# Performance work log

Hardware: AMD Instinct MI355X
Metric: run time of the kernel (lower is better)

Reference implementation:

```python
import jax, jax.numpy as jnp
from jax import lax
import numpy as np

NGF = 64
NZ = 16
B, H, W = 4, 224, 224
CTX = 512
HEADS = 1

def _gauss_kernel():
    ks, sigma = 3, 1.0
    ax = np.arange(ks, dtype=np.float32)
    xg, yg = np.meshgrid(ax, ax)
    mean = (ks - 1) / 2.0
    k = np.exp(-((xg - mean) ** 2 + (yg - mean) ** 2) / (2.0 * sigma ** 2)) / (2.0 * np.pi * sigma ** 2)
    k = k / k.sum()
    return jnp.asarray(np.tile(k[None, None], (3, 1, 1, 1)).astype(np.float32))

_GK = _gauss_kernel()  # depthwise gaussian blur kernel [3,1,3,3]

def _conv(x, w, stride=1, pad=0, groups=1):
    return lax.conv_general_dilated(x, w, (stride, stride), ((pad, pad), (pad, pad)),
                                    feature_group_count=groups,
                                    dimension_numbers=('NCHW', 'OIHW', 'NCHW'))

def _convT(x, w):
    # torch ConvTranspose2d(k=3, stride=2, padding=1, output_padding=1)
    wt = jnp.flip(w, (2, 3)).transpose(1, 0, 2, 3)
    return lax.conv_general_dilated(x, wt, (1, 1), ((1, 2), (1, 2)), lhs_dilation=(2, 2),
                                    dimension_numbers=('NCHW', 'OIHW', 'NCHW'))

def _refl(x, p):
    return jnp.pad(x, ((0, 0), (0, 0), (p, p), (p, p)), mode='reflect')

def _bn(x, g, b):
    # eval-mode BatchNorm2d with running_mean=0, running_var=1, eps=1e-5
    inv = g / np.float32(np.sqrt(1.0 + 1e-5))
    return x * inv[None, :, None, None] + b[None, :, None, None]

def _gn(x, g, b, groups=32, eps=1e-6):
    bsz, c, h, w = x.shape
    xr = x.reshape(bsz, groups, c // groups, h, w)
    m = xr.mean((2, 3, 4), keepdims=True)
    v = xr.var((2, 3, 4), keepdims=True)
    xr = (xr - m) / jnp.sqrt(v + eps)
    return xr.reshape(bsz, c, h, w) * g[None, :, None, None] + b[None, :, None, None]

def _ln(x, g, b, eps=1e-5):
    m = x.mean(-1, keepdims=True)
    v = x.var(-1, keepdims=True)
    return (x - m) / jnp.sqrt(v + eps) * g + b

def _attn(xq, ctx, wq, wk, wv, wo, bo, heads=HEADS):
    d = wq.shape[0] // heads
    scale = d ** -0.5
    q = xq @ wq.T
    k = ctx @ wk.T
    v = ctx @ wv.T
    bsz, n, _ = q.shape
    m = k.shape[1]
    q = q.reshape(bsz, n, heads, d).transpose(0, 2, 1, 3)
    k = k.reshape(bsz, m, heads, d).transpose(0, 2, 1, 3)
    v = v.reshape(bsz, m, heads, d).transpose(0, 2, 1, 3)
    sim = jnp.einsum('bhid,bhjd->bhij', q, k) * scale  # full score matrix, as in source
    a = jax.nn.softmax(sim, axis=-1)
    o = jnp.einsum('bhij,bhjd->bhid', a, v).transpose(0, 2, 1, 3).reshape(bsz, n, heads * d)
    return o @ wo.T + bo

def setup_inputs():
    keys = iter(jax.random.split(jax.random.key(0), 80))
    def rn(shape, s=0.02):
        return jax.random.normal(next(keys), shape, jnp.float32) * s
    c4 = NGF * 4
    d = {}
    d['input'] = jax.random.normal(next(keys), (B, 3, H, W), jnp.float32)
    d['cond'] = jax.random.normal(next(keys), (B, CTX), jnp.float32)
    d['sn_w'] = rn((NZ, CTX))
    d['sn_u'] = jax.random.normal(next(keys), (NZ,), jnp.float32)
    d['c1_w'] = rn((NGF, 3 + NZ, 7, 7))
    d['bn1_g'] = jnp.ones((NGF,)); d['bn1_b'] = jnp.zeros((NGF,))
    d['c2_w'] = rn((NGF * 2, NGF + NZ, 3, 3))
    d['bn2_g'] = jnp.ones((NGF * 2,)); d['bn2_b'] = jnp.zeros((NGF * 2,))
    d['c3_w'] = rn((c4, NGF * 2 + NZ, 3, 3))
    d['bn3_g'] = jnp.ones((c4,)); d['bn3_b'] = jnp.zeros((c4,))
    d['res_w'] = rn((6, 2, c4, c4, 3, 3))
    d['res_g'] = jnp.ones((6, 2, c4)); d['res_b'] = jnp.zeros((6, 2, c4))
    d['st_gn_g'] = jnp.ones((2, c4)); d['st_gn_b'] = jnp.zeros((2, c4))
    d['st_pin_w'] = rn((2, c4, c4, 1, 1)); d['st_pin_b'] = jnp.zeros((2, c4))
    d['st_q1'] = rn((2, c4, c4)); d['st_k1'] = rn((2, c4, c4)); d['st_v1'] = rn((2, c4, c4))
    d['st_o1w'] = rn((2, c4, c4)); d['st_o1b'] = jnp.zeros((2, c4))
    d['st_q2'] = rn((2, c4, c4)); d['st_k2'] = rn((2, c4, CTX)); d['st_v2'] = rn((2, c4, CTX))
    d['st_o2w'] = rn((2, c4, c4)); d['st_o2b'] = jnp.zeros((2, c4))
    d['st_ffp_w'] = rn((2, c4 * 8, c4)); d['st_ffp_b'] = jnp.zeros((2, c4 * 8))
    d['st_ffo_w'] = rn((2, c4, c4 * 4)); d['st_ffo_b'] = jnp.zeros((2, c4))
    for n in ('ln1', 'ln2', 'ln3'):
        d['st_' + n + 'g'] = jnp.ones((2, c4)); d['st_' + n + 'b'] = jnp.zeros((2, c4))
    d['st_pout_w'] = rn((2, c4, c4, 1, 1)); d['st_pout_b'] = jnp.zeros((2, c4))
    d['up1_w'] = rn((c4, NGF * 2, 3, 3))
    d['up1_g'] = jnp.ones((NGF * 2,)); d['up1_b'] = jnp.zeros((NGF * 2,))
    d['up2_w'] = rn((NGF * 2, NGF, 3, 3))
    d['up2_g'] = jnp.ones((NGF,)); d['up2_b'] = jnp.zeros((NGF,))
    d['cf_w'] = rn((3, NGF, 7, 7)); d['cf_b'] = jnp.zeros((3,))
    d['eps'] = 16
    return d

def reference(input, cond, eps, sn_w, sn_u, c1_w, bn1_g, bn1_b, c2_w, bn2_g, bn2_b, c3_w, bn3_g, bn3_b,
              res_w, res_g, res_b, st_gn_g, st_gn_b, st_pin_w, st_pin_b,
              st_q1, st_k1, st_v1, st_o1w, st_o1b, st_q2, st_k2, st_v2, st_o2w, st_o2b,
              st_ffp_w, st_ffp_b, st_ffo_w, st_ffo_b,
              st_ln1g, st_ln1b, st_ln2g, st_ln2b, st_ln3g, st_ln3b,
              st_pout_w, st_pout_b, up1_w, up1_g, up1_b, up2_w, up2_g, up2_b, cf_w, cf_b):
    relu = jax.nn.relu
    text_cond = cond[:, None, :]  # [B, 1, 512]
    # spectral-norm linear (one power iteration, u/v detached, as torch train-mode)
    v = sn_w.T @ sn_u
    v = v / (jnp.linalg.norm(v) + 1e-12)
    u = sn_w @ v
    u = u / (jnp.linalg.norm(u) + 1e-12)
    v = lax.stop_gradient(v); u = lax.stop_gradient(u)
    sigma = u @ (sn_w @ v)
    z = cond @ (sn_w / sigma).T  # [B, NZ]

    def tile_z(h, w):
        return jnp.broadcast_to(z[:, :, None, None], (z.shape[0], z.shape[1], h, w))

    x = jnp.concatenate([input, tile_z(input.shape[2], input.shape[3])], axis=1)
    x = relu(_bn(_conv(_refl(x, 3), c1_w), bn1_g, bn1_b))
    x = jnp.concatenate([x, tile_z(x.shape[2], x.shape[3])], axis=1)
    x = relu(_bn(_conv(x, c2_w, stride=2, pad=1), bn2_g, bn2_b))
    x = jnp.concatenate([x, tile_z(x.shape[2], x.shape[3])], axis=1)
    x = relu(_bn(_conv(x, c3_w, stride=2, pad=1), bn3_g, bn3_b))

    def resblock(x, w, g, b):
        h = relu(_bn(_conv(_refl(x, 1), w[0]), g[0], b[0]))  # dropout inactive (eval)
        h = _bn(_conv(_refl(h, 1), w[1]), g[1], b[1])
        return x + h

    def spatial_transformer(x, i):
        x_in = x
        x = _gn(x, st_gn_g[i], st_gn_b[i])
        x = _conv(x, st_pin_w[i]) + st_pin_b[i][None, :, None, None]
        bsz, c, h, w = x.shape
        t = x.reshape(bsz, c, h * w).transpose(0, 2, 1)  # b, hw, c
        h1 = _ln(t, st_ln1g[i], st_ln1b[i])
        t = _attn(h1, h1, st_q1[i], st_k1[i], st_v1[i], st_o1w[i], st_o1b[i]) + t
        h2 = _ln(t, st_ln2g[i], st_ln2b[i])
        t = _attn(h2, text_cond, st_q2[i], st_k2[i], st_v2[i], st_o2w[i], st_o2b[i]) + t
        h3 = _ln(t, st_ln3g[i], st_ln3b[i])
        p = h3 @ st_ffp_w[i].T + st_ffp_b[i]
        a, gate = jnp.split(p, 2, axis=-1)  # GEGLU
        t = (a * jax.nn.gelu(gate, approximate=False)) @ st_ffo_w[i].T + st_ffo_b[i] + t
        x = t.transpose(0, 2, 1).reshape(bsz, c, h, w)
        x = _conv(x, st_pout_w[i]) + st_pout_b[i][None, :, None, None]
        return x + x_in

    x = resblock(x, res_w[0], res_g[0], res_b[0])
    x = resblock(x, res_w[1], res_g[1], res_b[1])
    x = spatial_transformer(x, 0)
    x = resblock(x, res_w[2], res_g[2], res_b[2])
    x = resblock(x, res_w[3], res_g[3], res_b[3])
    x = spatial_transformer(x, 1)
    x = resblock(x, res_w[4], res_g[4], res_b[4])
    x = resblock(x, res_w[5], res_g[5], res_b[5])
    x = relu(_bn(_convT(x, up1_w), up1_g, up1_b))
    x = relu(_bn(_convT(x, up2_w), up2_g, up2_b))
    x = _conv(_refl(x, 3), cf_w) + cf_b[None, :, None, None]
    x = jnp.tanh(x)
    x = _conv(x, _GK, pad=1, groups=3)  # fixed gaussian blur
    return x * eps
```

## Files before the change

### kernel.cpp

```cpp
#include <hip/hip_runtime.h>
#include <math.h>

#ifndef DIVUP
#define DIVUP(a,b) (((a)+(b)-1)/(b))
#endif

typedef unsigned short ushort_t;
typedef __attribute__((ext_vector_type(8))) short v8s;
typedef __attribute__((ext_vector_type(4))) float v4f;

#define BB 4
#define NZ 16
#define C4 256
#define N56 3136
#define N112 12544
#define N224 50176

static const float BN_ALPHA = 0.99999500003749967f;

__device__ inline int refl_idx(int i, int n) {
  if (i < 0) i = -i;
  if (i >= n) i = 2 * n - 2 - i;
  return i;
}

__device__ inline void bsplit(float v, ushort_t& h, ushort_t& l) {
  unsigned b = __float_as_uint(v);
  unsigned r = (b + 0x7FFFu + ((b >> 16) & 1u)) & 0xFFFF0000u;
  h = (ushort_t)(r >> 16);
  float lo = v - __uint_as_float(r);
  unsigned bl_ = __float_as_uint(lo);
  unsigned rl = bl_ + 0x7FFFu + ((bl_ >> 16) & 1u);
  l = (ushort_t)(rl >> 16);
}

__device__ inline float blk_reduce_sum(float v, float* lds) {
  int t = threadIdx.x;
  lds[t] = v; __syncthreads();
  for (int s = 128; s > 0; s >>= 1) { if (t < s) lds[t] += lds[t + s]; __syncthreads(); }
  float r = lds[0]; __syncthreads();
  return r;
}
__device__ inline float blk_reduce_max(float v, float* lds) {
  int t = threadIdx.x;
  lds[t] = v; __syncthreads();
  for (int s = 128; s > 0; s >>= 1) { if (t < s) lds[t] = fmaxf(lds[t], lds[t + s]); __syncthreads(); }
  float r = lds[0]; __syncthreads();
  return r;
}

struct MArgs {
  const float* A; long long Am, Ak, Abatch;
  const float* Xp; long long Xbatch;
  const float* z;
  const ushort_t* Bh; const ushort_t* Bl;
  const float* Bf; long long Bbatch;
  long long Bstride;
  float* C; long long Cm, Cn, Cbatch;
  const float* scale; const float* bias;
  const float* resid; long long Rm, Rn, Rbatch;
  float alpha; int relu;
  int M, N;
  int ICP, NPH;
  int Cin;
  int KS, Hin, Win, Wout, stride, pad, reflect;
};

template<int AMODE, int BMN, int KSTEP, int BSPLIT>
__global__ __launch_bounds__(256, (BMN == 64 ? 3 : 2)) void mg_k(MArgs g) {
  constexpr int EPT  = BMN * KSTEP / 256;
  constexpr int MF   = BMN / 32;
  constexpr int LDSW = KSTEP + 8;
  constexpr int NSUB = KSTEP / 32;
  __shared__ __align__(16) ushort_t sAh[BMN * LDSW];
  __shared__ __align__(16) ushort_t sAl[BMN * LDSW];
  __shared__ __align__(16) ushort_t sBh[BMN * LDSW];
  __shared__ __align__(16) ushort_t sBl[BMN * LDSW];

  const int tid = threadIdx.x;
  const int b = blockIdx.z;
  const int m0 = blockIdx.y * BMN, n0 = blockIdx.x * BMN;
  const int lane = tid & 63, w = tid >> 6;
  const int wm = (w >> 1) * (MF * 16), wn = (w & 1) * (MF * 16);

  const int srow = tid & (BMN - 1);
  const int skoff = (tid / BMN) * EPT;

  int am = m0 + srow; if (am >= g.M) am = g.M - 1;
  int cy = 0, cx = 0;
  const float* Aptr;
  if (AMODE == 0) {
    Aptr = g.A + (long long)b * g.Abatch + (long long)am * g.Am;
  } else {
    cy = am / g.Wout; cx = am - cy * g.Wout;
    Aptr = g.Xp + (long long)b * g.Xbatch;
  }
  const int HW = g.Hin * g.Win;

  int bn = n0 + srow; if (bn >= g.N) bn = g.N - 1;
  const ushort_t* BhP = BSPLIT ? (g.Bh + (long long)bn * g.Bstride + skoff) : nullptr;
  const ushort_t* BlP = BSPLIT ? (g.Bl + (long long)bn * g.Bstride + skoff) : nullptr;
  const float* BfP = BSPLIT ? nullptr : (g.Bf + (long long)b * g.Bbatch + (long long)bn * g.Bstride + skoff);

  int ph = 0, ic0 = 0, pbase = 0;
  bool pvalid = true;
  int kglob = 0;

  float areg[EPT];
  ushort_t bregh[EPT], bregl[EPT];
  float bregf[EPT];

  auto fetchA = [&]() {
    if (AMODE == 0) {
      const float* Ap = Aptr + (long long)(kglob + skoff) * g.Ak;
      if (g.Ak == 1) {
        #pragma unroll
        for (int e = 0; e < EPT; ++e) areg[e] = Ap[e];
      } else {
        #pragma unroll
        for (int e = 0; e < EPT; ++e) areg[e] = Ap[(long long)e * g.Ak];
      }
      kglob += KSTEP;
    } else {
      if (ic0 == 0) {
        int ky = ph / g.KS, kx = ph - ky * g.KS;
        if (AMODE == 1) {
          int iy = cy * g.stride + ky - g.pad;
          int ix = cx * g.stride + kx - g.pad;
          if (g.reflect) {
            iy = refl_idx(iy, g.Hin); ix = refl_idx(ix, g.Win); pvalid = true;
          } else {
            pvalid = (iy >= 0 && iy < g.Hin && ix >= 0 && ix < g.Win);
            if (iy < 0) iy = 0; if (iy >= g.Hin) iy = g.Hin - 1;
            if (ix < 0) ix = 0; if (ix >= g.Win) ix = g.Win - 1;
          }
          pbase = iy * g.Win + ix;
        } else {
          int iy2 = cy + ky - 1, ix2 = cx + kx - 1;
          pvalid = (iy2 >= 0) && (ix2 >= 0) && !(iy2 & 1) && !(ix2 & 1);
          int iy = iy2 >> 1, ix = ix2 >> 1;
          if (pvalid && (iy >= g.Hin || ix >= g.Win)) pvalid = false;
          if (!pvalid) { iy = 0; ix = 0; }
          pbase = iy * g.Win + ix;
        }
      }
      #pragma unroll
      for (int e = 0; e < EPT; ++e) {
        int ic = ic0 + skoff + e;
        float v = 0.f;
        if (pvalid) {
          if (ic < g.Cin) v = Aptr[pbase + ic * HW];
          else if (g.z && ic < g.Cin + NZ) v = g.z[b * NZ + (ic - g.Cin)];
        }
        areg[e] = v;
      }
      ic0 += KSTEP; if (ic0 == g.ICP) { ic0 = 0; ++ph; }
    }
  };

  auto fetchB = [&](int k0) {
    if (BSPLIT) {
      #pragma unroll
      for (int e = 0; e < EPT; ++e) { bregh[e] = BhP[k0 + e]; bregl[e] = BlP[k0 + e]; }
    } else {
      #pragma unroll
      for (int e = 0; e < EPT; ++e) bregf[e] = BfP[k0 + e];
    }
  };

  v4f acc[MF][MF];
  #pragma unroll
  for (int i = 0; i < MF; ++i)
    #pragma unroll
    for (int j = 0; j < MF; ++j) acc[i][j] = (v4f)(0.f);

  const int nt = (g.ICP * g.NPH) / KSTEP;
  fetchA(); fetchB(0);

  const int fr = lane & 15, fk = (lane >> 4) * 8;

  for (int t = 0; t < nt; ++t) {
    __syncthreads();
    {
      ushort_t ah[EPT], al[EPT];
      #pragma unroll
      for (int e = 0; e < EPT; ++e) bsplit(areg[e], ah[e], al[e]);
      #pragma unroll
      for (int e = 0; e < EPT; ++e) { sAh[srow * LDSW + skoff + e] = ah[e]; sAl[srow * LDSW + skoff + e] = al[e]; }
      if (BSPLIT) {
        #pragma unroll
        for (int e = 0; e < EPT; ++e) { sBh[srow * LDSW + skoff + e] = bregh[e]; sBl[srow * LDSW + skoff + e] = bregl[e]; }
      } else {
        ushort_t bh[EPT], bl[EPT];
        #pragma unroll
        for (int e = 0; e < EPT; ++e) bsplit(bregf[e], bh[e], bl[e]);
        #pragma unroll
        for (int e = 0; e < EPT; ++e) { sBh[srow * LDSW + skoff + e] = bh[e]; sBl[srow * LDSW + skoff + e] = bl[e]; }
      }
    }
    __syncthreads();
    if (t + 1 < nt) { fetchA(); fetchB((t + 1) * KSTEP); }
    #pragma unroll
    for (int ks = 0; ks < NSUB; ++ks) {
      v8s fah[MF], fal[MF], fbh[MF], fbl[MF];
      #pragma unroll
      for (int i = 0; i < MF; ++i) {
        fah[i] = *(const v8s*)&sAh[(wm + i * 16 + fr) * LDSW + ks * 32 + fk];
        fal[i] = *(const v8s*)&sAl[(wm + i * 16 + fr) * LDSW + ks * 32 + fk];
        fbh[i] = *(const v8s*)&sBh[(wn + i * 16 + fr) * LDSW + ks * 32 + fk];
        fbl[i] = *(const v8s*)&sBl[(wn + i * 16 + fr) * LDSW + ks * 32 + fk];
      }
      #pragma unroll
      for (int i = 0; i < MF; ++i)
        #pragma unroll
        for (int j = 0; j < MF; ++j) {
          acc[i][j] = __builtin_amdgcn_mfma_f32_16x16x32_bf16(fah[i], fbh[j], acc[i][j], 0, 0, 0);
          acc[i][j] = __builtin_amdgcn_mfma_f32_16x16x32_bf16(fah[i], fbl[j], acc[i][j], 0, 0, 0);
          acc[i][j] = __builtin_amdgcn_mfma_f32_16x16x32_bf16(fal[i], fbh[j], acc[i][j], 0, 0, 0);
        }
    }
  }

  const int fq = lane >> 4;
  #pragma unroll
  for (int j = 0; j < MF; ++j) {
    int n = n0 + wn + j * 16 + fr;
    if (n >= g.N) continue;
    float sc = (g.scale ? g.scale[n] : 1.f) * g.alpha;
    float bs = g.bias ? g.bias[n] : 0.f;
    #pragma unroll
    for (int i = 0; i < MF; ++i) {
      int mb = m0 + wm + i * 16 + fq * 4;
      #pragma unroll
      for (int r = 0; r < 4; ++r) {
        int m = mb + r;
        if (m < g.M) {
          float v = acc[i][j][r] * sc + bs;
          if (g.resid) v += g.resid[(long long)b * g.Rbatch + (long long)m * g.Rm + (long long)n * g.Rn];
          if (g.relu) v = fmaxf(v, 0.f);
          g.C[(long long)b * g.Cbatch + (long long)m * g.Cm + (long long)n * g.Cn] = v;
        }
      }
    }
  }
}

__global__ void prep_lin_k(const float* __restrict__ src, ushort_t* __restrict__ dh,
                           ushort_t* __restrict__ dl, int tot) {
  int i = blockIdx.x * 256 + threadIdx.x;
  if (i >= tot) return;
  bsplit(src[i], dh[i], dl[i]);
}

__global__ void prep_conv_k(const float* __restrict__ src, ushort_t* __restrict__ dh,
                            ushort_t* __restrict__ dl, int N, int Cin, int ICP, int KS) {
  int idx = blockIdx.x * 256 + threadIdx.x;
  int K2 = KS * KS;
  int tot = N * K2 * ICP;
  if (idx >= tot) return;
  int ic = idx % ICP;
  int p = (idx / ICP) % K2;
  int n = idx / (ICP * K2);
  float v = (ic < Cin) ? src[(n * Cin + ic) * K2 + p] : 0.f;
  bsplit(v, dh[idx], dl[idx]);
}

__global__ void prep_convt_k(const float* __restrict__ src, ushort_t* __restrict__ dh,
                             ushort_t* __restrict__ dl, int Cin, int Cout) {
  int idx = blockIdx.x * 256 + threadIdx.x;
  int tot = Cout * 9 * Cin;
  if (idx >= tot) return;
  int ic = idx % Cin;
  int p = (idx / Cin) % 9;
  int o = idx / (9 * Cin);
  int ky = p / 3, kx = p % 3;
  float v = src[((ic * Cout + o) * 3 + (2 - ky)) * 3 + (2 - kx)];
  bsplit(v, dh[idx], dl[idx]);
}

__global__ __launch_bounds__(256) void spectral_z_k(const float* __restrict__ cond,
    const float* __restrict__ W, const float* __restrict__ u0, float* __restrict__ z) {
  __shared__ float v0[512];
  __shared__ float lds[256];
  __shared__ float wv[16];
  __shared__ float invs[2];
  int tid = threadIdx.x;
  float part = 0.f;
  #pragma unroll
  for (int r = 0; r < 2; ++r) {
    int j = tid + r * 256;
    float s = 0.f;
    #pragma unroll
    for (int i = 0; i < 16; ++i) s = fmaf(W[i * 512 + j], u0[i], s);
    v0[j] = s;
    part = fmaf(s, s, part);
  }
  float nv2 = blk_reduce_sum(part, lds);
  if (tid == 0) invs[0] = 1.f / (sqrtf(nv2) + 1e-12f);
  __syncthreads();
  float inv_nv = invs[0];
  {
    int i = tid >> 4, l = tid & 15;
    float s = 0.f;
    for (int jj = 0; jj < 32; ++jj) {
      int j = l + jj * 16;
      s = fmaf(W[i * 512 + j], v0[j], s);
    }
    lds[tid] = s; __syncthreads();
    if (l == 0) {
      float t = 0.f;
      for (int q = 0; q < 16; ++q) t += lds[(i << 4) + q];
      wv[i] = t * inv_nv;
    }
    __syncthreads();
    if (tid == 0) {
      float s2 = 0.f;
      for (int i2 = 0; i2 < 16; ++i2) s2 = fmaf(wv[i2], wv[i2], s2);
      float nw = sqrtf(s2);
      float sigma = s2 / (nw + 1e-12f);
      invs[1] = 1.f / sigma;
    }
    __syncthreads();
  }
  if (tid < 64) {
    int b = tid >> 4, i = tid & 15;
    float s = 0.f;
    for (int j = 0; j < 512; ++j) s = fmaf(cond[b * 512 + j], W[i * 512 + j], s);
    z[b * 16 + i] = s * invs[1];
  }
}

__global__ __launch_bounds__(256) void groupnorm_k(const float* __restrict__ x, float* __restrict__ out,
    const float* __restrict__ gam, const float* __restrict__ bet, int C, int HW, int cpg) {
  __shared__ float lds[256];
  int b = blockIdx.y, grp = blockIdx.x;
  long long base = ((long long)b * C + (long long)grp * cpg) * HW;
  int n = cpg * HW;
  float s = 0.f, s2 = 0.f;
  for (int i = threadIdx.x; i < n; i += 256) { float v = x[base + i]; s += v; s2 = fmaf(v, v, s2); }
  s  = blk_reduce_sum(s, lds);
  s2 = blk_reduce_sum(s2, lds);
  float m = s / (float)n;
  float var = s2 / (float)n - m * m;
  float rinv = 1.f / sqrtf(var + 1e-6f);
  for (int i = threadIdx.x; i < n; i += 256) {
    int c = grp * cpg + i / HW;
    out[base + i] = (x[base + i] - m) * rinv * gam[c] + bet[c];
  }
}

__global__ __launch_bounds__(256) void layernorm_k(const float* __restrict__ x, float* __restrict__ out,
    const float* __restrict__ g, const float* __restrict__ b) {
  __shared__ float lds[256];
  long long t = blockIdx.x;
  float v = x[t * 256 + threadIdx.x];
  float s  = blk_reduce_sum(v, lds);
  float s2 = blk_reduce_sum(v * v, lds);
  float m = s * (1.f / 256.f);
  float var = s2 * (1.f / 256.f) - m * m;
  float rinv = 1.f / sqrtf(var + 1e-5f);
  out[t * 256 + threadIdx.x] = (v - m) * rinv * g[threadIdx.x] + b[threadIdx.x];
}

__global__ __launch_bounds__(256) void softmax_k(float* __restrict__ S, float* __restrict__ den, int n) {
  __shared__ float lds[256];
  float* p = S + (long long)blockIdx.x * n;
  float mx = -3.4e38f;
  for (int i = threadIdx.x; i < n; i += 256) mx = fmaxf(mx, p[i]);
  mx = blk_reduce_max(mx, lds);
  float s = 0.f;
  for (int i = threadIdx.x; i < n; i += 256) { float e = __expf(p[i] - mx); p[i] = e; s += e; }
  s = blk_reduce_sum(s, lds);
  if (threadIdx.x == 0) den[blockIdx.x] = 1.f / s;
}

__global__ __launch_bounds__(256) void pv_reduce_k(const float* __restrict__ part,
    const float* __restrict__ den, float* __restrict__ out, int nchunk) {
  long long i = (long long)blockIdx.x * 256 + threadIdx.x;
  float s = 0.f;
  for (int c = 0; c < nchunk; ++c) s += part[(long long)c * 802816 + i];
  out[i] = s * den[i >> 8];
}

__global__ void geglu_k(float* __restrict__ p, int ntok) {
  int idx = blockIdx.x * 256 + threadIdx.x;
  if (idx >= ntok * 1024) return;
  int t = idx >> 10, j = idx & 1023;
  float a  = p[t * 2048 + j];
  float gt = p[t * 2048 + 1024 + j];
  float ge = 0.5f * gt * (1.f + erff(gt * 0.70710678118654752f));
  p[t * 2048 + j] = a * ge;
}

__global__ __launch_bounds__(256) void crossattn_vec_k(const float* __restrict__ cond,
    const float* __restrict__ v2w, const float* __restrict__ o2w, const float* __restrict__ o2b,
    float* __restrict__ o2buf) {
  __shared__ float kv[256];
  int b = blockIdx.x, oc = threadIdx.x;
  float s = 0.f;
  for (int j = 0; j < 512; ++j) s = fmaf(cond[b * 512 + j], v2w[oc * 512 + j], s);
  kv[oc] = s; __syncthreads();
  float o = o2b[oc];
  for (int ic = 0; ic < 256; ++ic) o = fmaf(kv[ic], o2w[oc * 256 + ic], o);
  o2buf[b * 256 + oc] = o;
}
__global__ void bcast_add_k(float* __restrict__ T, const float* __restrict__ o2buf, int ntok_per_b) {
  long long idx = (long long)blockIdx.x * 256 + threadIdx.x;
  int c = (int)(idx & 255);
  long long tb = idx >> 8;
  int b = (int)(tb / ntok_per_b);
  T[idx] += o2buf[b * 256 + c];
}

__global__ __launch_bounds__(256) void conv_final_k(const float* __restrict__ in,
    const float* __restrict__ w, const float* __restrict__ bias, float* __restrict__ out) {
  __shared__ float wl[3 * 64 * 49];
  for (int i = threadIdx.x; i < 3 * 64 * 49; i += 256) wl[i] = w[i];
  __syncthreads();
  int b = blockIdx.y;
  int p = blockIdx.x * 256 + threadIdx.x;
  int y = p / 224, x = p % 224;
  int iy[7], ix[7];
  #pragma unroll
  for (int t = 0; t < 7; ++t) {
    int a = y + t - 3; iy[t] = (a < 0) ? -a : ((a >= 224) ? 446 - a : a);
    int c = x + t - 3; ix[t] = (c < 0) ? -c : ((c >= 224) ? 446 - c : c);
  }
  float a0 = bias[0], a1 = bias[1], a2 = bias[2];
  for (int ic = 0; ic < 64; ++ic) {
    const float* ip = in + (long long)(b * 64 + ic) * N224;
    const float* w0 = &wl[(0 * 64 + ic) * 49];
    const float* w1 = &wl[(1 * 64 + ic) * 49];
    const float* w2 = &wl[(2 * 64 + ic) * 49];
    #pragma unroll
    for (int ky = 0; ky < 7; ++ky) {
      const float* rp = ip + iy[ky] * 224;
      #pragma unroll
      for (int kx = 0; kx < 7; ++kx) {
        float v = rp[ix[kx]];
        int t = ky * 7 + kx;
        a0 = fmaf(v, w0[t], a0);
        a1 = fmaf(v, w1[t], a1);
        a2 = fmaf(v, w2[t], a2);
      }
    }
  }
  long long ob = (long long)b * 3 * N224 + p;
  out[ob]            = tanhf(a0);
  out[ob + N224]     = tanhf(a1);
  out[ob + 2 * N224] = tanhf(a2);
}

__global__ void blur_k(const float* __restrict__ x, float* __restrict__ out, const int* __restrict__ epsp) {
  int idx = blockIdx.x * 256 + threadIdx.x;
  int xp = idx % 224;
  int y  = (idx / 224) % 224;
  int bc = idx / N224;
  const float* p = x + (long long)bc * N224;
  const float kc = 0.20417996f, k1 = 0.12384140f, k2 = 0.07511360f;
  float s = 0.f;
  #pragma unroll
  for (int dy = -1; dy <= 1; ++dy) {
    int yy = y + dy;
    if (yy < 0 || yy >= 224) continue;
    #pragma unroll
    for (int dx = -1; dx <= 1; ++dx) {
      int xx = xp + dx;
      if (xx < 0 || xx >= 224) continue;
      float wgt = (dy == 0 && dx == 0) ? kc : ((dy != 0 && dx != 0) ? k2 : k1);
      s = fmaf(p[yy * 224 + xx], wgt, s);
    }
  }
  out[idx] = s * (float)epsp[0];
}

static inline MArgs MA() { MArgs g = {}; g.alpha = 1.f; return g; }

template<int AMODE, int BMN, int KSTEP, int BSPLIT>
static inline void mgl(hipStream_t s, const MArgs& g, int zb) {
  dim3 grid(DIVUP(g.N, BMN), DIVUP(g.M, BMN), zb);
  mg_k<AMODE, BMN, KSTEP, BSPLIT><<<grid, 256, 0, s>>>(g);
}

extern "C" void kernel_launch(void* const* d_in, const int* in_sizes, int n_in,
                              void* d_out, int out_size, void* d_ws, size_t ws_size,
                              hipStream_t stream) {
  (void)in_sizes; (void)n_in; (void)out_size; (void)ws_size;
  const float* input = (const float*)d_in[0];
  const float* cond  = (const float*)d_in[1];
  const float* sn_w  = (const float*)d_in[2];
  const float* sn_u  = (const float*)d_in[3];
  const float* c1_w  = (const float*)d_in[4];
  const float* bn1_g = (const float*)d_in[5];
  const float* bn1_b = (const float*)d_in[6];
  const float* c2_w  = (const float*)d_in[7];
  const float* bn2_g = (const float*)d_in[8];
  const float* bn2_b = (const float*)d_in[9];
  const float* c3_w  = (const float*)d_in[10];
  const float* bn3_g = (const float*)d_in[11];
  const float* bn3_b = (const float*)d_in[12];
  const float* res_w = (const float*)d_in[13];
  const float* res_g = (const float*)d_in[14];
  const float* res_b = (const float*)d_in[15];
  const float* gn_g  = (const float*)d_in[16];
  const float* gn_b  = (const float*)d_in[17];
  const float* pin_w = (const float*)d_in[18];
  const float* pin_b = (const float*)d_in[19];
  const float* q1w   = (const float*)d_in[20];
  const float* k1w   = (const float*)d_in[21];
  const float* v1w   = (const float*)d_in[22];
  const float* o1w   = (const float*)d_in[23];
  const float* o1b   = (const float*)d_in[24];
  const float* v2w   = (const float*)d_in[27];
  const float* o2w   = (const float*)d_in[28];
  const float* o2b   = (const float*)d_in[29];
  const float* ffpw  = (const float*)d_in[30];
  const float* ffpb  = (const float*)d_in[31];
  const float* ffow  = (const float*)d_in[32];
  const float* ffob  = (const float*)d_in[33];
  const float* ln1g  = (const float*)d_in[34];
  const float* ln1b  = (const float*)d_in[35];
  const float* ln3g  = (const float*)d_in[38];
  const float* ln3b  = (const float*)d_in[39];
  const float* poutw = (const float*)d_in[40];
  const float* poutb = (const float*)d_in[41];
  const float* up1w  = (const float*)d_in[42];
  const float* up1g  = (const float*)d_in[43];
  const float* up1b  = (const float*)d_in[44];
  const float* up2w  = (const float*)d_in[45];
  const float* up2g  = (const float*)d_in[46];
  const float* up2b  = (const float*)d_in[47];
  const float* cfw   = (const float*)d_in[48];
  const float* cfb   = (const float*)d_in[49];
  const int*   epsp  = (const int*)d_in[50];

  const long long S56 = (long long)C4 * N56;

  float* A1   = (float*)d_ws;
  float* A2   = A1 + 12845056;
  float* SIMb = A2 + 6422528;
  float* X    = SIMb + 9834496;
  float* T    = X + 3211264;
  float* Hb   = T + 3211264;
  float* Qb   = Hb + 3211264;
  float* Kb   = Qb + 3211264;
  float* Vt   = Kb + 3211264;
  ushort_t* TFWh = (ushort_t*)(Vt + 3211264);
  ushort_t* TFWl = TFWh + 2359296;
  float* Zb = (float*)(TFWl + 2359296);
  float* O2 = Zb + 64;
  float* Sden = O2 + 1024;
  ushort_t* RESW = (ushort_t*)A1;
  ushort_t* SC = (ushort_t*)SIMb;
  ushort_t* c1h = SC,            * c1l = c1h + 100352;
  ushort_t* c2h = c1l + 100352,  * c2l = c2h + 110592;
  ushort_t* c3h = c2l + 110592,  * c3l = c3h + 368640;
  ushort_t* u1h = c3l + 368640,  * u1l = u1h + 294912;
  ushort_t* u2h = u1l + 294912,  * u2l = u2h + 73728;
  float* CF = SIMb + 948224;
  float* FF = A2;
  float* PVP = A2;

  const int TFQ = 0, TFK = 65536, TFV = 131072, TFO1 = 196608, TFPIN = 262144,
            TFPOUT = 327680, TFFFP = 393216, TFFFO = 917504, TFSZ = 1179648;

  spectral_z_k<<<1, 256, 0, stream>>>(cond, sn_w, sn_u, Zb);
  prep_conv_k<<<DIVUP(64 * 49 * 32, 256), 256, 0, stream>>>(c1_w, c1h, c1l, 64, 19, 32, 7);
  prep_conv_k<<<DIVUP(128 * 9 * 96, 256), 256, 0, stream>>>(c2_w, c2h, c2l, 128, 80, 96, 3);
  prep_conv_k<<<DIVUP(256 * 9 * 160, 256), 256, 0, stream>>>(c3_w, c3h, c3l, 256, 144, 160, 3);
  for (int i = 0; i < 2; ++i) {
    ushort_t* bh = TFWh + i * TFSZ; ushort_t* bl = TFWl + i * TFSZ;
    prep_lin_k<<<256, 256, 0, stream>>>(q1w  + (size_t)i * 65536, bh + TFQ,   bl + TFQ,   65536);
    prep_lin_k<<<256, 256, 0, stream>>>(k1w  + (size_t)i * 65536, bh + TFK,   bl + TFK,   65536);
    prep_lin_k<<<256, 256, 0, stream>>>(v1w  + (size_t)i * 65536, bh + TFV,   bl + TFV,   65536);
    prep_lin_k<<<256, 256, 0, stream>>>(o1w  + (size_t)i * 65536, bh + TFO1,  bl + TFO1,  65536);
    prep_lin_k<<<256, 256, 0, stream>>>(pin_w + (size_t)i * 65536, bh + TFPIN, bl + TFPIN, 65536);
    prep_lin_k<<<256, 256, 0, stream>>>(poutw + (size_t)i * 65536, bh + TFPOUT, bl + TFPOUT, 65536);
    prep_lin_k<<<2048, 256, 0, stream>>>(ffpw + (size_t)i * 524288, bh + TFFFP, bl + TFFFP, 524288);
    prep_lin_k<<<1024, 256, 0, stream>>>(ffow + (size_t)i * 262144, bh + TFFFO, bl + TFFFO, 262144);
  }

  {
    MArgs g = MA();
    g.Xp = input; g.Xbatch = 3LL * N224; g.z = Zb; g.Cin = 3;
    g.Bh = c1h; g.Bl = c1l; g.Bstride = 1568;
    g.C = A1; g.Cm = 1; g.Cn = N224; g.Cbatch = 64LL * N224;
    g.scale = bn1_g; g.bias = bn1_b; g.alpha = BN_ALPHA; g.relu = 1;
    g.M = N224; g.N = 64; g.ICP = 32; g.NPH = 49;
    g.KS = 7; g.Hin = 224; g.Win = 224; g.Wout = 224; g.stride = 1; g.pad = 3; g.reflect = 1;
    mgl<1, 64, 32, 1>(stream, g, BB);
  }
  {
    MArgs g = MA();
    g.Xp = A1; g.Xbatch = 64LL * N224; g.z = Zb; g.Cin = 64;
    g.Bh = c2h; g.Bl = c2l; g.Bstride = 864;
    g.C = A2; g.Cm = 1; g.Cn = N112; g.Cbatch = 128LL * N112;
    g.scale = bn2_g; g.bias = bn2_b; g.alpha = BN_ALPHA; g.relu = 1;
    g.M = N112; g.N = 128; g.ICP = 96; g.NPH = 9;
    g.KS = 3; g.Hin = 224; g.Win = 224; g.Wout = 112; g.stride = 2; g.pad = 1; g.reflect = 0;
    mgl<1, 64, 32, 1>(stream, g, BB);
  }
  for (int j = 0; j < 12; ++j) {
    ushort_t* bh = RESW + (size_t)j * 1179648;
    prep_conv_k<<<DIVUP(256 * 9 * 256, 256), 256, 0, stream>>>(
        res_w + (size_t)j * 589824, bh, bh + 589824, 256, 256, 256, 3);
  }
  {
    MArgs g = MA();
    g.Xp = A2; g.Xbatch = 128LL * N112; g.z = Zb; g.Cin = 128;
    g.Bh = c3h; g.Bl = c3l; g.Bstride = 1440;
    g.C = X; g.Cm = 1; g.Cn = N56; g.Cbatch = S56;
    g.scale = bn3_g; g.bias = bn3_b; g.alpha = BN_ALPHA; g.relu = 1;
    g.M = N56; g.N = 256; g.ICP = 160; g.NPH = 9;
    g.KS = 3; g.Hin = 112; g.Win = 112; g.Wout = 56; g.stride = 2; g.pad = 1; g.reflect = 0;
    mgl<1, 64, 32, 1>(stream, g, BB);
  }

  auto resconv = [&](int j, const float* src, float* dst, int relu, const float* resid) {
    MArgs g = MA();
    g.Xp = src; g.Xbatch = S56; g.Cin = 256;
    ushort_t* bh = RESW + (size_t)j * 1179648;
    g.Bh = bh; g.Bl = bh + 589824; g.Bstride = 2304;
    g.C = dst; g.Cm = 1; g.Cn = N56; g.Cbatch = S56;
    g.scale = res_g + j * 256; g.bias = res_b + j * 256; g.alpha = BN_ALPHA; g.relu = relu;
    if (resid) { g.resid = resid; g.Rm = 1; g.Rn = N56; g.Rbatch = S56; }
    g.M = N56; g.N = 256; g.ICP = 256; g.NPH = 9;
    g.KS = 3; g.Hin = 56; g.Win = 56; g.Wout = 56; g.stride = 1; g.pad = 1; g.reflect = 1;
    mgl<1, 64, 64, 1>(stream, g, BB);
  };
  auto resblock = [&](int r) {
    resconv(r * 2, X, Hb, 1, nullptr);
    resconv(r * 2 + 1, Hb, X, 0, X);
  };

  auto lin = [&](int i, int woff, const float* A, long long Am, long long Ak, long long Ab,
                 float* C, long long Cm, long long Cn, long long Cb,
                 const float* bias, const float* resid, long long Rm, long long Rn, long long Rb,
                 int M, int N, int K, float alpha, int zb) {
    MArgs g = MA();
    g.A = A; g.Am = Am; g.Ak = Ak; g.Abatch = Ab;
    g.Bh = TFWh + i * TFSZ + woff; g.Bl = TFWl + i * TFSZ + woff; g.Bstride = K;
    g.C = C; g.Cm = Cm; g.Cn = Cn; g.Cbatch = Cb;
    g.bias = bias;
    if (resid) { g.resid = resid; g.Rm = Rm; g.Rn = Rn; g.Rbatch = Rb; }
    g.alpha = alpha; g.M = M; g.N = N; g.ICP = K; g.NPH = 1;
    mgl<0, 64, 64, 1>(stream, g, zb);
  };

  auto transformer = [&](int i) {
    groupnorm_k<<<dim3(32, BB), 256, 0, stream>>>(X, Hb, gn_g + i * 256, gn_b + i * 256, 256, N56, 8);
    lin(i, TFPIN, Hb, 1, N56, S56, T, 256, 1, S56, pin_b + i * 256,
        nullptr, 0, 0, 0, N56, 256, 256, 1.f, BB);
    layernorm_k<<<BB * N56, 256, 0, stream>>>(T, Hb, ln1g + i * 256, ln1b + i * 256);
    lin(i, TFQ, Hb, 256, 1, S56, Qb, 256, 1, S56, nullptr, nullptr, 0, 0, 0, N56, 256, 256, 1.f, BB);
    lin(i, TFK, Hb, 256, 1, S56, Kb, 256, 1, S56, nullptr, nullptr, 0, 0, 0, N56, 256, 256, 1.f, BB);
    lin(i, TFV, Hb, 256, 1, S56, Vt, 1, N56, S56, nullptr, nullptr, 0, 0, 0, N56, 256, 256, 1.f, BB);
    for (int b = 0; b < BB; ++b) {
      {
        MArgs g = MA();
        g.A = Qb + (size_t)b * S56; g.Am = 256; g.Ak = 1; g.Abatch = 0;
        g.Bf = Kb + (size_t)b * S56; g.Bstride = 256; g.Bbatch = 0;
        g.C = SIMb; g.Cm = N56; g.Cn = 1; g.Cbatch = 0;
        g.alpha = 0.0625f; g.M = N56; g.N = N56; g.ICP = 256; g.NPH = 1;
        mgl<0, 128, 32, 0>(stream, g, 1);
      }
      softmax_k<<<N56, 256, 0, stream>>>(SIMb, Sden, N56);
      {
        MArgs g = MA();
        g.A = SIMb; g.Am = N56; g.Ak = 1; g.Abatch = 448;
        g.Bf = Vt + (size_t)b * S56; g.Bstride = N56; g.Bbatch = 448;
        g.C = PVP; g.Cm = 256; g.Cn = 1; g.Cbatch = 802816;
        g.M = N56; g.N = 256; g.ICP = 448; g.NPH = 1;
        mgl<0, 64, 64, 0>(stream, g, 7);
      }
      pv_reduce_k<<<3136, 256, 0, stream>>>(PVP, Sden, Hb + (size_t)b * S56, 7);
    }
    lin(i, TFO1, Hb, 256, 1, S56, T, 256, 1, S56, o1b + i * 256,
        T, 256, 1, S56, N56, 256, 256, 1.f, BB);
    crossattn_vec_k<<<BB, 256, 0, stream>>>(cond, v2w + (size_t)i * 131072,
                                            o2w + (size_t)i * 65536, o2b + i * 256, O2);
    bcast_add_k<<<BB * N56, 256, 0, stream>>>(T, O2, N56);
    layernorm_k<<<BB * N56, 256, 0, stream>>>(T, Hb, ln3g + i * 256, ln3b + i * 256);
    for (int b = 0; b < BB; ++b) {
      lin(i, TFFFP, Hb + (size_t)b * S56, 256, 1, 0, FF, 2048, 1, 0, ffpb + i * 2048,
          nullptr, 0, 0, 0, N56, 2048, 256, 1.f, 1);
      geglu_k<<<DIVUP(N56 * 1024, 256), 256, 0, stream>>>(FF, N56);
      lin(i, TFFFO, FF, 2048, 1, 0, T + (size_t)b * S56, 256, 1, 0, ffob + i * 256,
          T + (size_t)b * S56, 256, 1, 0, N56, 256, 1024, 1.f, 1);
    }
    lin(i, TFPOUT, T, 256, 1, S56, X, 1, N56, S56, poutb + i * 256,
        X, 1, N56, S56, N56, 256, 256, 1.f, BB);
  };

  resblock(0); resblock(1);
  transformer(0);
  resblock(2); resblock(3);
  transformer(1);
  resblock(4); resblock(5);

  prep_convt_k<<<DIVUP(128 * 9 * 256, 256), 256, 0, stream>>>(up1w, u1h, u1l, 256, 128);
  prep_convt_k<<<DIVUP(64 * 9 * 128, 256), 256, 0, stream>>>(up2w, u2h, u2l, 128, 64);

  {
    MArgs g = MA();
    g.Xp = X; g.Xbatch = S56; g.Cin = 256;
    g.Bh = u1h; g.Bl = u1l; g.Bstride = 2304;
    g.C = A2; g.Cm = 1; g.Cn = N112; g.Cbatch = 128LL * N112;
    g.scale = up1g; g.bias = up1b; g.alpha = BN_ALPHA; g.relu = 1;
    g.M = N112; g.N = 128; g.ICP = 256; g.NPH = 9;
    g.KS = 3; g.Hin = 56; g.Win = 56; g.Wout = 112;
    mgl<2, 64, 64, 1>(stream, g, BB);
  }
  {
    MArgs g = MA();
    g.Xp = A2; g.Xbatch = 128LL * N112; g.Cin = 128;
    g.Bh = u2h; g.Bl = u2l; g.Bstride = 1152;
    g.C = A1; g.Cm = 1; g.Cn = N224; g.Cbatch = 64LL * N224;
    g.scale = up2g; g.bias = up2b; g.alpha = BN_ALPHA; g.relu = 1;
    g.M = N224; g.N = 64; g.ICP = 128; g.NPH = 9;
    g.KS = 3; g.Hin = 112; g.Win = 112; g.Wout = 224;
    mgl<2, 64, 64, 1>(stream, g, BB);
  }

  conv_final_k<<<dim3(N224 / 256, BB), 256, 0, stream>>>(A1, cfw, cfb, CF);
  blur_k<<<DIVUP(BB * 3 * N224, 256), 256, 0, stream>>>(CF, (float*)d_out, epsp);
}
```

Measured before the change: 8.741 ms.

## Double-buffer the MFMA GEMM kernel, vectorize loads, and move final conv onto it

The templated GEMM kernel is collapsed to a single 64x64 tile with K-step 32. Its LDS staging is now double-buffered with a two-deep register prefetch, so only one barrier per iteration remains. Global and LDS accesses use float4/v8s vector loads and stores. The scalar 7x7 final conv kernel is replaced by the implicit-GEMM path, with a tanh epilogue (relu==2) and prepped split-bf16 weights. The risks are more LDS per block, the loss of the larger 128 tile for the attention QK GEMM, and wasted work on the N=3 final conv, since a 64-wide N tile is mostly padding.

```diff
diff --git a/kernel.cpp b/kernel.cpp
--- a/kernel.cpp
+++ b/kernel.cpp
@@ -66,25 +66,22 @@
   int KS, Hin, Win, Wout, stride, pad, reflect;
 };
 
-template<int AMODE, int BMN, int KSTEP, int BSPLIT>
-__global__ __launch_bounds__(256, (BMN == 64 ? 3 : 2)) void mg_k(MArgs g) {
-  constexpr int EPT  = BMN * KSTEP / 256;
-  constexpr int MF   = BMN / 32;
-  constexpr int LDSW = KSTEP + 8;
-  constexpr int NSUB = KSTEP / 32;
-  __shared__ __align__(16) ushort_t sAh[BMN * LDSW];
-  __shared__ __align__(16) ushort_t sAl[BMN * LDSW];
-  __shared__ __align__(16) ushort_t sBh[BMN * LDSW];
-  __shared__ __align__(16) ushort_t sBl[BMN * LDSW];
+template<int AMODE, int BSPLIT>
+__global__ __launch_bounds__(256, 3) void mg_k(MArgs g) {
+  constexpr int BMN = 64, EPT = 8, LDSW = 40;
+  __shared__ __align__(16) ushort_t sAh[2][BMN * LDSW];
+  __shared__ __align__(16) ushort_t sAl[2][BMN * LDSW];
+  __shared__ __align__(16) ushort_t sBh[2][BMN * LDSW];
+  __shared__ __align__(16) ushort_t sBl[2][BMN * LDSW];
 
   const int tid = threadIdx.x;
   const int b = blockIdx.z;
   const int m0 = blockIdx.y * BMN, n0 = blockIdx.x * BMN;
   const int lane = tid & 63, w = tid >> 6;
-  const int wm = (w >> 1) * (MF * 16), wn = (w & 1) * (MF * 16);
-
-  const int srow = tid & (BMN - 1);
-  const int skoff = (tid / BMN) * EPT;
+  const int wm = (w >> 1) * 32, wn = (w & 1) * 32;
+
+  const int srow = tid & 63;
+  const int skoff = (tid >> 6) * EPT;
 
   int am = m0 + srow; if (am >= g.M) am = g.M - 1;
   int cy = 0, cx = 0;
@@ -107,20 +104,22 @@
   int kglob = 0;
 
   float areg[EPT];
-  ushort_t bregh[EPT], bregl[EPT];
+  v8s bregh, bregl;
   float bregf[EPT];
 
   auto fetchA = [&]() {
     if (AMODE == 0) {
       const float* Ap = Aptr + (long long)(kglob + skoff) * g.Ak;
       if (g.Ak == 1) {
-        #pragma unroll
-        for (int e = 0; e < EPT; ++e) areg[e] = Ap[e];
+        float4 a0 = *(const float4*)Ap;
+        float4 a1 = *(const float4*)(Ap + 4);
+        areg[0] = a0.x; areg[1] = a0.y; areg[2] = a0.z; areg[3] = a0.w;
+        areg[4] = a1.x; areg[5] = a1.y; areg[6] = a1.z; areg[7] = a1.w;
       } else {
         #pragma unroll
         for (int e = 0; e < EPT; ++e) areg[e] = Ap[(long long)e * g.Ak];
       }
-      kglob += KSTEP;
+      kglob += 32;
     } else {
       if (ic0 == 0) {
         int ky = ph / g.KS, kx = ph - ky * g.KS;
@@ -154,82 +153,88 @@
         }
         areg[e] = v;
       }
-      ic0 += KSTEP; if (ic0 == g.ICP) { ic0 = 0; ++ph; }
+      ic0 += 32; if (ic0 == g.ICP) { ic0 = 0; ++ph; }
     }
   };
 
   auto fetchB = [&](int k0) {
     if (BSPLIT) {
+      bregh = *(const v8s*)(BhP + k0);
+      bregl = *(const v8s*)(BlP + k0);
+    } else {
+      float4 f0 = *(const float4*)(BfP + k0);
+      float4 f1 = *(const float4*)(BfP + k0 + 4);
+      bregf[0] = f0.x; bregf[1] = f0.y; bregf[2] = f0.z; bregf[3] = f0.w;
+      bregf[4] = f1.x; bregf[5] = f1.y; bregf[6] = f1.z; bregf[7] = f1.w;
+    }
+  };
+
+  auto stash = [&](int bi) {
+    ushort_t ah[EPT], al[EPT];
+    #pragma unroll
+    for (int e = 0; e < EPT; ++e) bsplit(areg[e], ah[e], al[e]);
+    *(v8s*)&sAh[bi][srow * LDSW + skoff] = *(v8s*)ah;
+    *(v8s*)&sAl[bi][srow * LDSW + skoff] = *(v8s*)al;
+    if (BSPLIT) {
+      *(v8s*)&sBh[bi][srow * LDSW + skoff] = bregh;
+      *(v8s*)&sBl[bi][srow * LDSW + skoff] = bregl;
+    } else {
+      ushort_t bh[EPT], bl[EPT];
       #pragma unroll
-      for (int e = 0; e < EPT; ++e) { bregh[e] = BhP[k0 + e]; bregl[e] = BlP[k0 + e]; }
-    } else {
+      for (int e = 0; e < EPT; ++e) bsplit(bregf[e], bh[e], bl[e]);
+      *(v8s*)&sBh[bi][srow * LDSW + skoff] = *(v8s*)bh;
+      *(v8s*)&sBl[bi][srow * LDSW + skoff] = *(v8s*)bl;
+    }
+  };
+
+  v4f acc[2][2];
+  #pragma unroll
+  for (int i = 0; i < 2; ++i)
+    #pragma unroll
+    for (int j = 0; j < 2; ++j) acc[i][j] = (v4f)(0.f);
+
+  const int nt = (g.ICP * g.NPH) / 32;
+  const int fr = lane & 15, fk = (lane >> 4) * 8;
+
+  fetchA(); fetchB(0);
+  stash(0);
+  if (nt > 1) { fetchA(); fetchB(32); }
+  __syncthreads();
+
+  for (int t = 0; t < nt; ++t) {
+    const int cur = t & 1;
+    if (t + 1 < nt) stash(cur ^ 1);
+    if (t + 2 < nt) { fetchA(); fetchB((t + 2) * 32); }
+    {
+      v8s fah[2], fal[2], fbh[2], fbl[2];
       #pragma unroll
-      for (int e = 0; e < EPT; ++e) bregf[e] = BfP[k0 + e];
-    }
-  };
-
-  v4f acc[MF][MF];
-  #pragma unroll
-  for (int i = 0; i < MF; ++i)
-    #pragma unroll
-    for (int j = 0; j < MF; ++j) acc[i][j] = (v4f)(0.f);
-
-  const int nt = (g.ICP * g.NPH) / KSTEP;
-  fetchA(); fetchB(0);
-
-  const int fr = lane & 15, fk = (lane >> 4) * 8;
-
-  for (int t = 0; t < nt; ++t) {
-    __syncthreads();
-    {
-      ushort_t ah[EPT], al[EPT];
-      #pragma unroll
-      for (int e = 0; e < EPT; ++e) bsplit(areg[e], ah[e], al[e]);
-      #pragma unroll
-      for (int e = 0; e < EPT; ++e) { sAh[srow * LDSW + skoff + e] = ah[e]; sAl[srow * LDSW + skoff + e] = al[e]; }
-      if (BSPLIT) {
-        #pragma unroll
-        for (int e = 0; e < EPT; ++e) { sBh[srow * LDSW + skoff + e] = bregh[e]; sBl[srow * LDSW + skoff + e] = bregl[e]; }
-      } else {
-        ushort_t bh[EPT], bl[EPT];
-        #pragma unroll
-        for (int e = 0; e < EPT; ++e) bsplit(bregf[e], bh[e], bl[e]);
-        #pragma unroll
-        for (int e = 0; e < EPT; ++e) { sBh[srow * LDSW + skoff + e] = bh[e]; sBl[srow * LDSW + skoff + e] = bl[e]; }
-      }
-    }
-    __syncthreads();
-    if (t + 1 < nt) { fetchA(); fetchB((t + 1) * KSTEP); }
-    #pragma unroll
-    for (int ks = 0; ks < NSUB; ++ks) {
-      v8s fah[MF], fal[MF], fbh[MF], fbl[MF];
-      #pragma unroll
-      for (int i = 0; i < MF; ++i) {
-        fah[i] = *(const v8s*)&sAh[(wm + i * 16 + fr) * LDSW + ks * 32 + fk];
-        fal[i] = *(const v8s*)&sAl[(wm + i * 16 + fr) * LDSW + ks * 32 + fk];
-        fbh[i] = *(const v8s*)&sBh[(wn + i * 16 + fr) * LDSW + ks * 32 + fk];
-        fbl[i] = *(const v8s*)&sBl[(wn + i * 16 + fr) * LDSW + ks * 32 + fk];
+      for (int i = 0; i < 2; ++i) {
+        fah[i] = *(const v8s*)&sAh[cur][(wm + i * 16 + fr) * LDSW + fk];
+        fal[i] = *(const v8s*)&sAl[cur][(wm + i * 16 + fr) * LDSW + fk];
+        fbh[i] = *(const v8s*)&sBh[cur][(wn + i * 16 + fr) * LDSW + fk];
+        fbl[i] = *(const v8s*)&sBl[cur][(wn + i * 16 + fr) * LDSW + fk];
       }
       #pragma unroll
-      for (int i = 0; i < MF; ++i)
+      for (int i = 0; i < 2; ++i)
         #pragma unroll
-        for (int j = 0; j < MF; ++j) {
+        for (int j = 0; j < 2; ++j) {
           acc[i][j] = __builtin_amdgcn_mfma_f32_16x16x32_bf16(fah[i], fbh[j], acc[i][j], 0, 0, 0);
           acc[i][j] = __builtin_amdgcn_mfma_f32_16x16x32_bf16(fah[i], fbl[j], acc[i][j], 0, 0, 0);
           acc[i][j] = __builtin_amdgcn_mfma_f32_16x16x32_bf16(fal[i], fbh[j], acc[i][j], 0, 0, 0);
         }
     }
+    __syncthreads();
   }
 
   const int fq = lane >> 4;
   #pragma unroll
-  for (int j = 0; j < MF; ++j) {
+  for (int j = 0; j < 2; ++j) {
     int n = n0 + wn + j * 16 + fr;
     if (n >= g.N) continue;
     float sc = (g.scale ? g.scale[n] : 1.f) * g.alpha;
     float bs = g.bias ? g.bias[n] : 0.f;
     #pragma unroll
-    for (int i = 0; i < MF; ++i) {
+    for (int i = 0; i < 2; ++i) {
       int mb = m0 + wm + i * 16 + fq * 4;
       #pragma unroll
       for (int r = 0; r < 4; ++r) {
@@ -237,7 +242,8 @@
         if (m < g.M) {
           float v = acc[i][j][r] * sc + bs;
           if (g.resid) v += g.resid[(long long)b * g.Rbatch + (long long)m * g.Rm + (long long)n * g.Rn];
-          if (g.relu) v = fmaxf(v, 0.f);
+          if (g.relu == 1) v = fmaxf(v, 0.f);
+          else if (g.relu == 2) v = tanhf(v);
           g.C[(long long)b * g.Cbatch + (long long)m * g.Cm + (long long)n * g.Cn] = v;
         }
       }
@@ -410,45 +416,6 @@
   long long tb = idx >> 8;
   int b = (int)(tb / ntok_per_b);
   T[idx] += o2buf[b * 256 + c];
-}
-
-__global__ __launch_bounds__(256) void conv_final_k(const float* __restrict__ in,
-    const float* __restrict__ w, const float* __restrict__ bias, float* __restrict__ out) {
-  __shared__ float wl[3 * 64 * 49];
-  for (int i = threadIdx.x; i < 3 * 64 * 49; i += 256) wl[i] = w[i];
-  __syncthreads();
-  int b = blockIdx.y;
-  int p = blockIdx.x * 256 + threadIdx.x;
-  int y = p / 224, x = p % 224;
-  int iy[7], ix[7];
-  #pragma unroll
-  for (int t = 0; t < 7; ++t) {
-    int a = y + t - 3; iy[t] = (a < 0) ? -a : ((a >= 224) ? 446 - a : a);
-    int c = x + t - 3; ix[t] = (c < 0) ? -c : ((c >= 224) ? 446 - c : c);
-  }
-  float a0 = bias[0], a1 = bias[1], a2 = bias[2];
-  for (int ic = 0; ic < 64; ++ic) {
-    const float* ip = in + (long long)(b * 64 + ic) * N224;
-    const float* w0 = &wl[(0 * 64 + ic) * 49];
-    const float* w1 = &wl[(1 * 64 + ic) * 49];
-    const float* w2 = &wl[(2 * 64 + ic) * 49];
-    #pragma unroll
-    for (int ky = 0; ky < 7; ++ky) {
-      const float* rp = ip + iy[ky] * 224;
-      #pragma unroll
-      for (int kx = 0; kx < 7; ++kx) {
-        float v = rp[ix[kx]];
-        int t = ky * 7 + kx;
-        a0 = fmaf(v, w0[t], a0);
-        a1 = fmaf(v, w1[t], a1);
-        a2 = fmaf(v, w2[t], a2);
-      }
-    }
-  }
-  long long ob = (long long)b * 3 * N224 + p;
-  out[ob]            = tanhf(a0);
-  out[ob + N224]     = tanhf(a1);
-  out[ob + 2 * N224] = tanhf(a2);
 }
 
 __global__ void blur_k(const float* __restrict__ x, float* __restrict__ out, const int* __restrict__ epsp) {
@@ -476,10 +443,10 @@
 
 static inline MArgs MA() { MArgs g = {}; g.alpha = 1.f; return g; }
 
-template<int AMODE, int BMN, int KSTEP, int BSPLIT>
+template<int AMODE, int BSPLIT>
 static inline void mgl(hipStream_t s, const MArgs& g, int zb) {
-  dim3 grid(DIVUP(g.N, BMN), DIVUP(g.M, BMN), zb);
-  mg_k<AMODE, BMN, KSTEP, BSPLIT><<<grid, 256, 0, s>>>(g);
+  dim3 grid(DIVUP(g.N, 64), DIVUP(g.M, 64), zb);
+  mg_k<AMODE, BSPLIT><<<grid, 256, 0, s>>>(g);
 }
 
 extern "C" void kernel_launch(void* const* d_in, const int* in_sizes, int n_in,
@@ -557,7 +524,8 @@
   ushort_t* c3h = c2l + 110592,  * c3l = c3h + 368640;
   ushort_t* u1h = c3l + 368640,  * u1l = u1h + 294912;
   ushort_t* u2h = u1l + 294912,  * u2l = u2h + 73728;
-  float* CF = SIMb + 948224;
+  ushort_t* cfh = u2l + 73728,   * cfl = cfh + 9408;
+  float* CF = SIMb + 960000;
   float* FF = A2;
   float* PVP = A2;
 
@@ -588,7 +556,7 @@
     g.scale = bn1_g; g.bias = bn1_b; g.alpha = BN_ALPHA; g.relu = 1;
     g.M = N224; g.N = 64; g.ICP = 32; g.NPH = 49;
     g.KS = 7; g.Hin = 224; g.Win = 224; g.Wout = 224; g.stride = 1; g.pad = 3; g.reflect = 1;
-    mgl<1, 64, 32, 1>(stream, g, BB);
+    mgl<1, 1>(stream, g, BB);
   }
   {
     MArgs g = MA();
@@ -598,7 +566,7 @@
     g.scale = bn2_g; g.bias = bn2_b; g.alpha = BN_ALPHA; g.relu = 1;
     g.M = N112; g.N = 128; g.ICP = 96; g.NPH = 9;
     g.KS = 3; g.Hin = 224; g.Win = 224; g.Wout = 112; g.stride = 2; g.pad = 1; g.reflect = 0;
-    mgl<1, 64, 32, 1>(stream, g, BB);
+    mgl<1, 1>(stream, g, BB);
   }
   for (int j = 0; j < 12; ++j) {
     ushort_t* bh = RESW + (size_t)j * 1179648;
@@ -613,7 +581,7 @@
     g.scale = bn3_g; g.bias = bn3_b; g.alpha = BN_ALPHA; g.relu = 1;
     g.M = N56; g.N = 256; g.ICP = 160; g.NPH = 9;
     g.KS = 3; g.Hin = 112; g.Win = 112; g.Wout = 56; g.stride = 2; g.pad = 1; g.reflect = 0;
-    mgl<1, 64, 32, 1>(stream, g, BB);
+    mgl<1, 1>(stream, g, BB);
   }
 
   auto resconv = [&](int j, const float* src, float* dst, int relu, const float* resid) {
@@ -626,7 +594,7 @@
     if (resid) { g.resid = resid; g.Rm = 1; g.Rn = N56; g.Rbatch = S56; }
     g.M = N56; g.N = 256; g.ICP = 256; g.NPH = 9;
     g.KS = 3; g.Hin = 56; g.Win = 56; g.Wout = 56; g.stride = 1; g.pad = 1; g.reflect = 1;
-    mgl<1, 64, 64, 1>(stream, g, BB);
+    mgl<1, 1>(stream, g, BB);
   };
   auto resblock = [&](int r) {
     resconv(r * 2, X, Hb, 1, nullptr);
@@ -644,7 +612,7 @@
     g.bias = bias;
     if (resid) { g.resid = resid; g.Rm = Rm; g.Rn = Rn; g.Rbatch = Rb; }
     g.alpha = alpha; g.M = M; g.N = N; g.ICP = K; g.NPH = 1;
-    mgl<0, 64, 64, 1>(stream, g, zb);
+    mgl<0, 1>(stream, g, zb);
   };
 
   auto transformer = [&](int i) {
@@ -662,7 +630,7 @@
         g.Bf = Kb + (size_t)b * S56; g.Bstride = 256; g.Bbatch = 0;
         g.C = SIMb; g.Cm = N56; g.Cn = 1; g.Cbatch = 0;
         g.alpha = 0.0625f; g.M = N56; g.N = N56; g.ICP = 256; g.NPH = 1;
-        mgl<0, 128, 32, 0>(stream, g, 1);
+        mgl<0, 0>(stream, g, 1);
       }
       softmax_k<<<N56, 256, 0, stream>>>(SIMb, Sden, N56);
       {
@@ -671,7 +639,7 @@
         g.Bf = Vt + (size_t)b * S56; g.Bstride = N56; g.Bbatch = 448;
         g.C = PVP; g.Cm = 256; g.Cn = 1; g.Cbatch = 802816;
         g.M = N56; g.N = 256; g.ICP = 448; g.NPH = 1;
-        mgl<0, 64, 64, 0>(stream, g, 7);
+        mgl<0, 0>(stream, g, 7);
       }
       pv_reduce_k<<<3136, 256, 0, stream>>>(PVP, Sden, Hb + (size_t)b * S56, 7);
     }
@@ -700,6 +668,7 @@
 
   prep_convt_k<<<DIVUP(128 * 9 * 256, 256), 256, 0, stream>>>(up1w, u1h, u1l, 256, 128);
   prep_convt_k<<<DIVUP(64 * 9 * 128, 256), 256, 0, stream>>>(up2w, u2h, u2l, 128, 64);
+  prep_conv_k<<<DIVUP(3 * 49 * 64, 256), 256, 0, stream>>>(cfw, cfh, cfl, 3, 64, 64, 7);
 
   {
     MArgs g = MA();
@@ -709,7 +678,7 @@
     g.scale = up1g; g.bias = up1b; g.alpha = BN_ALPHA; g.relu = 1;
     g.M = N112; g.N = 128; g.ICP = 256; g.NPH = 9;
     g.KS = 3; g.Hin = 56; g.Win = 56; g.Wout = 112;
-    mgl<2, 64, 64, 1>(stream, g, BB);
+    mgl<2, 1>(stream, g, BB);
   }
   {
     MArgs g = MA();
@@ -719,9 +688,17 @@
     g.scale = up2g; g.bias = up2b; g.alpha = BN_ALPHA; g.relu = 1;
     g.M = N224; g.N = 64; g.ICP = 128; g.NPH = 9;
     g.KS = 3; g.Hin = 112; g.Win = 112; g.Wout = 224;
-    mgl<2, 64, 64, 1>(stream, g, BB);
-  }
-
-  conv_final_k<<<dim3(N224 / 256, BB), 256, 0, stream>>>(A1, cfw, cfb, CF);
+    mgl<2, 1>(stream, g, BB);
+  }
+  {
+    MArgs g = MA();
+    g.Xp = A1; g.Xbatch = 64LL * N224; g.Cin = 64;
+    g.Bh = cfh; g.Bl = cfl; g.Bstride = 3136;
+    g.C = CF; g.Cm = 1; g.Cn = N224; g.Cbatch = 3LL * N224;
+    g.bias = cfb; g.relu = 2;
+    g.M = N224; g.N = 3; g.ICP = 64; g.NPH = 49;
+    g.KS = 7; g.Hin = 224; g.Win = 224; g.Wout = 224; g.stride = 1; g.pad = 3; g.reflect = 1;
+    mgl<1, 1>(stream, g, BB);
+  }
   blur_k<<<DIVUP(BB * 3 * N224, 256), 256, 0, stream>>>(CF, (float*)d_out, epsp);
 }
```

Measured after the change: 7.456 ms. 1.17x faster.
